# Kernel optimization log

Hardware: AMD Instinct MI355X
Metric: run time of the kernel (lower is better)

Reference implementation:

```python
import jax, jax.numpy as jnp
import numpy as np
import math

V = 32000      # vocab_size
CTX = 1025     # context_length (S = CTX-1)
L = 4          # num_layers
D = 1024       # hidden_dim
H = 16         # heads
DH = D // H    # head_dim
FF = 4 * D
B = 2
PAD = 3        # padding_idx / tokenizer.pad_id()


def setup_inputs() -> dict:
    key = jax.random.key(0)
    ks = jax.random.split(key, 16)
    g = lambda k, shape: jax.random.normal(k, shape, dtype=jnp.float32) * 0.02
    text = jax.random.randint(ks[0], (B, CTX), 0, V)
    emb = g(ks[1], (V, D)).at[PAD].set(0.0)   # nn.Embedding with padding_idx=3
    u = g(ks[2], (H, DH))
    v = g(ks[3], (H, DH))
    Wq = g(ks[4], (L, D, D))
    Wk = g(ks[5], (L, D, D))
    Wv = g(ks[6], (L, D, D))
    Wr = g(ks[7], (L, D, D))
    Wfc = g(ks[8], (L, D, D))
    bfc = jnp.zeros((L, D), jnp.float32)
    ln1g = jnp.ones((L, D), jnp.float32); ln1b = jnp.zeros((L, D), jnp.float32)
    ln2g = jnp.ones((L, D), jnp.float32); ln2b = jnp.zeros((L, D), jnp.float32)
    W1 = g(ks[9], (L, D, FF)); b1 = jnp.zeros((L, FF), jnp.float32)
    W2 = g(ks[10], (L, FF, D)); b2 = jnp.zeros((L, D), jnp.float32)
    lnfg = jnp.ones((D,), jnp.float32); lnfb = jnp.zeros((D,), jnp.float32)
    Wlm = g(ks[11], (D, V)); blm = jnp.zeros((V,), jnp.float32)
    return dict(text=text, emb=emb, u=u, v=v, Wq=Wq, Wk=Wk, Wv=Wv, Wr=Wr,
                Wfc=Wfc, bfc=bfc, ln1g=ln1g, ln1b=ln1b, ln2g=ln2g, ln2b=ln2b,
                W1=W1, b1=b1, W2=W2, b2=b2, lnfg=lnfg, lnfb=lnfb, Wlm=Wlm, blm=blm)


def _ln(x, g, b, eps=1e-5):
    m = x.mean(-1, keepdims=True)
    va = ((x - m) ** 2).mean(-1, keepdims=True)
    return (x - m) / jnp.sqrt(va + eps) * g + b


def _rel_shift(x):
    # Transformer-XL relative shift: pad a zero column, reshape, drop first row.
    b, h, s, r = x.shape
    xp = jnp.pad(x, ((0, 0), (0, 0), (0, 0), (1, 0)))     # (b,h,s,r+1)
    xp = xp.reshape(b, h, r + 1, s)
    return xp[:, :, 1:, :].reshape(b, h, s, r)


def _forward(text, emb, u, v, Wq, Wk, Wv, Wr, Wfc, bfc, ln1g, ln1b, ln2g, ln2b,
             W1, b1, W2, b2, lnfg, lnfb, Wlm, blm):
    ip = text[:, :-1]                 # ip_text = text[:, :-1]
    S = ip.shape[1]
    x = emb[ip]                       # (B,S,D)
    # PositionalEmbedding over Transformer-XL positions [S-1 .. 0]
    pos = jnp.arange(S - 1, -1, -1, dtype=jnp.float32)
    inv_freq = 1.0 / (10000.0 ** (jnp.arange(0, D, 2, dtype=jnp.float32) / D))
    sinu = pos[:, None] * inv_freq[None, :]
    rel = jnp.concatenate([jnp.sin(sinu), jnp.cos(sinu)], axis=-1)  # (S,D)
    # get_mask: causal triu OR pad-token rows
    causal = jnp.triu(jnp.ones((S, S), dtype=bool), 1)
    pad = (ip == PAD)
    mask = (pad[:, :, None] | causal[None]) [:, None, :, :]        # (B,1,S,S)
    full_row = mask.all(-1, keepdims=True)                          # fully-masked rows -> NaN-fill 0
    scale = 1.0 / math.sqrt(DH)
    for l in range(L):
        xn = _ln(x, ln1g[l], ln1b[l])
        q = (xn @ Wq[l]).reshape(B, S, H, DH).transpose(0, 2, 1, 3)   # (B,H,S,DH)
        k = (xn @ Wk[l]).reshape(B, S, H, DH).transpose(0, 2, 1, 3)
        vv = (xn @ Wv[l]).reshape(B, S, H, DH).transpose(0, 2, 1, 3)
        r = (rel @ Wr[l]).reshape(S, H, DH).transpose(1, 0, 2)        # (H,S,DH)
        term_AC = jnp.einsum('bhqd,bhkd->bhqk', q + u[None, :, None, :], k)
        term_BD = jnp.einsum('bhqd,hkd->bhqk', q + v[None, :, None, :], r)
        term_BD = _rel_shift(term_BD)
        scores = (term_AC + term_BD) * scale
        scores = jnp.where(mask, -1e30, scores)
        aw = jax.nn.softmax(scores, axis=-1)
        aw = jnp.where(full_row, 0.0, aw)                              # NaN -> 0 masking
        o = jnp.einsum('bhqk,bhkd->bhqd', aw, vv).transpose(0, 2, 1, 3).reshape(B, S, D)
        o = o @ Wfc[l] + bfc[l] + xn                                   # fc(out) + attn-input residual
        x = x + o                                                      # block residual
        h = _ln(x, ln2g[l], ln2b[l])
        f = jax.nn.gelu(h @ W1[l] + b1[l])
        f = jax.nn.gelu(f @ W2[l] + b2[l])
        x = x + f
    xf = _ln(x, lnfg, lnfb)
    return xf @ Wlm + blm                                              # (B,S,V) logits


def reference(text, emb, u, v, Wq, Wk, Wv, Wr, Wfc, bfc, ln1g, ln1b, ln2g, ln2b,
              W1, b1, W2, b2, lnfg, lnfb, Wlm, blm):
    return _forward(text, emb, u, v, Wq, Wk, Wv, Wr, Wfc, bfc, ln1g, ln1b,
                    ln2g, ln2b, W1, b1, W2, b2, lnfg, lnfb, Wlm, blm)
```

## Files before the change

kernel.cpp:

```cpp
#include <hip/hip_runtime.h>
#include <stdint.h>

#define S_ 1024
#define D_ 1024
#define H_ 16
#define DH_ 64
#define FF_ 4096
#define B_ 2
#define V_ 32000
#define CTX_ 1025
#define PAD_ 3

typedef unsigned short u16;
typedef __attribute__((ext_vector_type(8))) short bf16x8;
typedef __attribute__((ext_vector_type(4))) float f32x4;

enum { EPI_BF16 = 0, EPI_QKV = 1, EPI_FC = 2, EPI_GELU_BF16 = 3, EPI_GELU_RES = 4, EPI_BIAS_F32 = 5 };

__device__ __forceinline__ u16 f2bf(float f) {
  unsigned u = __float_as_uint(f);
  return (u16)((u + 0x7FFFu + ((u >> 16) & 1u)) >> 16);
}

__device__ __forceinline__ float bf2f(u16 v) {
  return __uint_as_float(((unsigned)v) << 16);
}

__device__ __forceinline__ float gelu_f(float x) {
  float t = tanhf(0.7978845608028654f * (x + 0.044715f * x * x * x));
  return 0.5f * x * (1.0f + t);
}

__device__ __forceinline__ void glds16(const void* g, void* l) {
  __builtin_amdgcn_global_load_lds(
      (const __attribute__((address_space(1))) unsigned int*)g,
      (__attribute__((address_space(3))) unsigned int*)l,
      16, 0, 0);
}

__global__ __launch_bounds__(256) void embed_gather(const int* __restrict__ text,
                                                    const float* __restrict__ emb,
                                                    float* __restrict__ x) {
  int row = blockIdx.x;
  int b = row >> 10, s = row & 1023;
  int id = text[b * CTX_ + s];
  float4 v = ((const float4*)(emb + (size_t)id * D_))[threadIdx.x];
  ((float4*)(x + (size_t)row * D_))[threadIdx.x] = v;
}

__global__ __launch_bounds__(256) void rel_enc(u16* __restrict__ rel) {
  int i = blockIdx.x;
  float pos = (float)(S_ - 1 - i);
  for (int t = threadIdx.x; t < 512; t += 256) {
    float invf = exp2f(-(float)t * (13.287712379549449f / 512.0f));
    float ang = pos * invf;
    rel[(size_t)i * D_ + t] = f2bf(sinf(ang));
    rel[(size_t)i * D_ + 512 + t] = f2bf(cosf(ang));
  }
}

__global__ __launch_bounds__(256) void wconv_t(const float* __restrict__ src,
                                               u16* __restrict__ dst, int K, int N) {
  src += (size_t)blockIdx.z * K * N;
  dst += (size_t)blockIdx.z * K * N;
  __shared__ float tile[32][33];
  int n0 = blockIdx.x * 32, k0 = blockIdx.y * 32;
  for (int idx = threadIdx.x; idx < 1024; idx += 256) {
    int r = idx >> 5, c = idx & 31;
    tile[r][c] = src[(size_t)(k0 + r) * N + n0 + c];
  }
  __syncthreads();
  for (int idx = threadIdx.x; idx < 1024; idx += 256) {
    int r = idx >> 5, c = idx & 31;
    dst[(size_t)(n0 + r) * K + k0 + c] = f2bf(tile[c][r]);
  }
}

__global__ __launch_bounds__(256) void wconv4_k(const float* __restrict__ sq,
                                                const float* __restrict__ sk,
                                                const float* __restrict__ sv,
                                                const float* __restrict__ sf,
                                                u16* __restrict__ dqkv,
                                                u16* __restrict__ dfc) {
  const int z = blockIdx.z;
  const float* src = (z == 0) ? sq : (z == 1) ? sk : (z == 2) ? sv : sf;
  u16* dst = (z < 3) ? dqkv + (size_t)z * 1024 * 1024 : dfc;
  __shared__ float tile[32][33];
  int n0 = blockIdx.x * 32, k0 = blockIdx.y * 32;
  for (int idx = threadIdx.x; idx < 1024; idx += 256) {
    int r = idx >> 5, c = idx & 31;
    tile[r][c] = src[(size_t)(k0 + r) * 1024 + n0 + c];
  }
  __syncthreads();
  for (int idx = threadIdx.x; idx < 1024; idx += 256) {
    int r = idx >> 5, c = idx & 31;
    dst[(size_t)(n0 + r) * 1024 + k0 + c] = f2bf(tile[c][r]);
  }
}

__global__ __launch_bounds__(256) void layernorm_k(const float* __restrict__ x,
                                                   const float* __restrict__ g,
                                                   const float* __restrict__ bb,
                                                   float* __restrict__ outf,
                                                   u16* __restrict__ outb) {
  int row = blockIdx.x, tid = threadIdx.x;
  const float* xr = x + (size_t)row * D_;
  float4 v = ((const float4*)xr)[tid];
  float s = v.x + v.y + v.z + v.w;
  float s2 = v.x * v.x + v.y * v.y + v.z * v.z + v.w * v.w;
  __shared__ float red[8];
#pragma unroll
  for (int off = 32; off > 0; off >>= 1) { s += __shfl_xor(s, off); s2 += __shfl_xor(s2, off); }
  if ((tid & 63) == 0) { red[tid >> 6] = s; red[4 + (tid >> 6)] = s2; }
  __syncthreads();
  s = red[0] + red[1] + red[2] + red[3];
  s2 = red[4] + red[5] + red[6] + red[7];
  float mean = s * (1.0f / D_);
  float var = s2 * (1.0f / D_) - mean * mean;
  float rstd = rsqrtf(var + 1e-5f);
  float4 gv = ((const float4*)g)[tid];
  float4 bv = ((const float4*)bb)[tid];
  float y0 = (v.x - mean) * rstd * gv.x + bv.x;
  float y1 = (v.y - mean) * rstd * gv.y + bv.y;
  float y2 = (v.z - mean) * rstd * gv.z + bv.z;
  float y3 = (v.w - mean) * rstd * gv.w + bv.w;
  if (outf) ((float4*)(outf + (size_t)row * D_))[tid] = make_float4(y0, y1, y2, y3);
  ((ushort4*)(outb + (size_t)row * D_))[tid] = make_ushort4(f2bf(y0), f2bf(y1), f2bf(y2), f2bf(y3));
}

__device__ __forceinline__ void epi_one(int mode, float v, int row, int col, int ldc,
                                        void* C0p, void* C1p, void* C2p, void* C3p,
                                        const float* bias0, const float* bias1,
                                        const float* res0) {
  if (mode == EPI_QKV) {
    int seg = col >> 10, c = col & 1023;
    size_t idx = (size_t)row * 1024 + c;
    if (seg == 0) {
      ((u16*)C0p)[idx] = f2bf(v + bias0[c]);
      ((u16*)C1p)[idx] = f2bf(v + bias1[c]);
    } else if (seg == 1) {
      ((u16*)C2p)[idx] = f2bf(v);
    } else {
      ((u16*)C3p)[idx] = f2bf(v);
    }
    return;
  }
  size_t idx = (size_t)row * ldc + col;
  float b0 = bias0 ? bias0[col] : 0.0f;
  if (mode == EPI_BF16) {
    ((u16*)C0p)[idx] = f2bf(v);
  } else if (mode == EPI_FC) {
    float* C0 = (float*)C0p;
    C0[idx] = C0[idx] + v + b0 + res0[idx];
  } else if (mode == EPI_GELU_BF16) {
    ((u16*)C0p)[idx] = f2bf(gelu_f(v + b0));
  } else if (mode == EPI_GELU_RES) {
    float* C0 = (float*)C0p;
    C0[idx] = C0[idx] + gelu_f(v + b0);
  } else {
    ((float*)C0p)[idx] = v + b0;
  }
}

__global__ __launch_bounds__(256) void gemm_bt(const u16* __restrict__ A,
                                               const u16* __restrict__ Bt,
                                               int M, int N, int K,
                                               void* __restrict__ C0p, void* __restrict__ C1p,
                                               void* __restrict__ C2p, void* __restrict__ C3p,
                                               const float* __restrict__ bias0,
                                               const float* __restrict__ bias1,
                                               const float* __restrict__ res0,
                                               int ldc, int mode) {
  __shared__ u16 lA[128 * 64];
  __shared__ u16 lB[128 * 64];
  const int tid = threadIdx.x;
  const int wave = tid >> 6, lane = tid & 63;
  unsigned gx = gridDim.x, gy = gridDim.y;
  unsigned nwg = gx * gy;
  unsigned bx = blockIdx.x, by = blockIdx.y;
  if ((nwg & 7u) == 0u) {
    unsigned lin = by * gx + bx;
    unsigned v = (lin & 7u) * (nwg >> 3) + (lin >> 3);
    bx = v / gy;
    by = v - bx * gy;
  }
  const int i0 = by * 128, j0 = bx * 128;
  const int wm = wave & 1, wn = wave >> 1;
  const int m_lane = lane & 15, quad = lane >> 4;

  f32x4 acc[4][4] = {};

  const u16* Ab = A + (size_t)i0 * K;
  const u16* Bb = Bt + (size_t)j0 * K;
  const int sr = lane >> 3;
  const int sc = ((lane & 7) ^ sr) * 8;

  for (int k0 = 0; k0 < K; k0 += 64) {
#pragma unroll
    for (int c = 0; c < 4; c++) {
      int row = wave * 32 + c * 8 + sr;
      glds16(Ab + (size_t)row * K + k0 + sc, lA + (size_t)(wave * 32 + c * 8) * 64);
      glds16(Bb + (size_t)row * K + k0 + sc, lB + (size_t)(wave * 32 + c * 8) * 64);
    }
    __syncthreads();
    bf16x8 af[4], bfr[4];
#pragma unroll
    for (int t = 0; t < 4; t++) {
      int ra = wm * 64 + t * 16 + m_lane;
      int rb_ = wn * 64 + t * 16 + m_lane;
      af[t]  = *(const bf16x8*)(lA + ra * 64 + ((quad ^ (ra & 7)) * 8));
      bfr[t] = *(const bf16x8*)(lB + rb_ * 64 + ((quad ^ (rb_ & 7)) * 8));
    }
#pragma unroll
    for (int mt = 0; mt < 4; mt++)
#pragma unroll
      for (int nt = 0; nt < 4; nt++)
        acc[mt][nt] = __builtin_amdgcn_mfma_f32_16x16x32_bf16(af[mt], bfr[nt], acc[mt][nt], 0, 0, 0);
#pragma unroll
    for (int t = 0; t < 4; t++) {
      int ra = wm * 64 + t * 16 + m_lane;
      int rb_ = wn * 64 + t * 16 + m_lane;
      af[t]  = *(const bf16x8*)(lA + ra * 64 + (((4 + quad) ^ (ra & 7)) * 8));
      bfr[t] = *(const bf16x8*)(lB + rb_ * 64 + (((4 + quad) ^ (rb_ & 7)) * 8));
    }
#pragma unroll
    for (int mt = 0; mt < 4; mt++)
#pragma unroll
      for (int nt = 0; nt < 4; nt++)
        acc[mt][nt] = __builtin_amdgcn_mfma_f32_16x16x32_bf16(af[mt], bfr[nt], acc[mt][nt], 0, 0, 0);
    __syncthreads();
  }

#pragma unroll
  for (int mt = 0; mt < 4; mt++) {
#pragma unroll
    for (int nt = 0; nt < 4; nt++) {
      int col = j0 + wn * 64 + nt * 16 + m_lane;
#pragma unroll
      for (int r = 0; r < 4; r++) {
        int row = i0 + wm * 64 + mt * 16 + quad * 4 + r;
        epi_one(mode, acc[mt][nt][r], row, col, ldc, C0p, C1p, C2p, C3p, bias0, bias1, res0);
      }
    }
  }
}

__global__ __launch_bounds__(256) void gemm_bt64(const u16* __restrict__ A,
                                                 const u16* __restrict__ Bt,
                                                 int M, int N, int K,
                                                 void* __restrict__ C0p, void* __restrict__ C1p,
                                                 void* __restrict__ C2p, void* __restrict__ C3p,
                                                 const float* __restrict__ bias0,
                                                 const float* __restrict__ bias1,
                                                 const float* __restrict__ res0,
                                                 int ldc, int mode) {
  __shared__ u16 lA[64 * 64];
  __shared__ u16 lB[128 * 64];
  const int tid = threadIdx.x;
  const int wave = tid >> 6, lane = tid & 63;
  unsigned gx = gridDim.x, gy = gridDim.y;
  unsigned nwg = gx * gy;
  unsigned bx = blockIdx.x, by = blockIdx.y;
  if ((nwg & 7u) == 0u) {
    unsigned lin = by * gx + bx;
    unsigned v = (lin & 7u) * (nwg >> 3) + (lin >> 3);
    by = v / gx;
    bx = v - by * gx;
  }
  const int i0 = by * 64, j0 = bx * 128;
  const int m_lane = lane & 15, quad = lane >> 4;

  f32x4 acc[4][2] = {};

  const u16* Ab = A + (size_t)i0 * K;
  const u16* Bb = Bt + (size_t)j0 * K;
  const int sr = lane >> 3;
  const int sc = ((lane & 7) ^ sr) * 8;

  for (int k0 = 0; k0 < K; k0 += 64) {
#pragma unroll
    for (int c = 0; c < 2; c++) {
      int row = wave * 16 + c * 8 + sr;
      glds16(Ab + (size_t)row * K + k0 + sc, lA + (size_t)(wave * 16 + c * 8) * 64);
    }
#pragma unroll
    for (int c = 0; c < 4; c++) {
      int row = wave * 32 + c * 8 + sr;
      glds16(Bb + (size_t)row * K + k0 + sc, lB + (size_t)(wave * 32 + c * 8) * 64);
    }
    __syncthreads();
    bf16x8 af[4], bfr[2];
#pragma unroll
    for (int t = 0; t < 4; t++) {
      int ra = t * 16 + m_lane;
      af[t] = *(const bf16x8*)(lA + ra * 64 + ((quad ^ (ra & 7)) * 8));
    }
#pragma unroll
    for (int t = 0; t < 2; t++) {
      int rb_ = wave * 32 + t * 16 + m_lane;
      bfr[t] = *(const bf16x8*)(lB + rb_ * 64 + ((quad ^ (rb_ & 7)) * 8));
    }
#pragma unroll
    for (int mt = 0; mt < 4; mt++)
#pragma unroll
      for (int nt = 0; nt < 2; nt++)
        acc[mt][nt] = __builtin_amdgcn_mfma_f32_16x16x32_bf16(af[mt], bfr[nt], acc[mt][nt], 0, 0, 0);
#pragma unroll
    for (int t = 0; t < 4; t++) {
      int ra = t * 16 + m_lane;
      af[t] = *(const bf16x8*)(lA + ra * 64 + (((4 + quad) ^ (ra & 7)) * 8));
    }
#pragma unroll
    for (int t = 0; t < 2; t++) {
      int rb_ = wave * 32 + t * 16 + m_lane;
      bfr[t] = *(const bf16x8*)(lB + rb_ * 64 + (((4 + quad) ^ (rb_ & 7)) * 8));
    }
#pragma unroll
    for (int mt = 0; mt < 4; mt++)
#pragma unroll
      for (int nt = 0; nt < 2; nt++)
        acc[mt][nt] = __builtin_amdgcn_mfma_f32_16x16x32_bf16(af[mt], bfr[nt], acc[mt][nt], 0, 0, 0);
    __syncthreads();
  }

#pragma unroll
  for (int mt = 0; mt < 4; mt++) {
#pragma unroll
    for (int nt = 0; nt < 2; nt++) {
      int col = j0 + wave * 32 + nt * 16 + m_lane;
#pragma unroll
      for (int r = 0; r < 4; r++) {
        int row = i0 + mt * 16 + quad * 4 + r;
        epi_one(mode, acc[mt][nt][r], row, col, ldc, C0p, C1p, C2p, C3p, bias0, bias1, res0);
      }
    }
  }
}

__global__ __launch_bounds__(256) void attn_score(const u16* __restrict__ qu,
                                                  const u16* __restrict__ qv,
                                                  const u16* __restrict__ kk,
                                                  const u16* __restrict__ rb,
                                                  float* __restrict__ scores) {
  __shared__ u16 sBD[64][132];
  const int cIdx = blockIdx.x, bh = blockIdx.y;
  int ti = (int)((sqrtf(8.0f * (float)cIdx + 1.0f) - 1.0f) * 0.5f);
  while ((ti + 1) * (ti + 2) / 2 <= cIdx) ti++;
  while (ti * (ti + 1) / 2 > cIdx) ti--;
  const int tj = cIdx - ti * (ti + 1) / 2;
  const int b = bh >> 4, h = bh & 15;
  const int tid = threadIdx.x, wave = tid >> 6, lane = tid & 63;
  const int m_lane = lane & 15, quad = lane >> 4;
  const int i0 = ti * 64, j0 = tj * 64;
  const int T0 = 15 - (ti - tj);
  const bool hasT1 = (T0 < 15);

  const u16* Qu = qu + ((size_t)(b * S_ + i0 + wave * 16 + m_lane)) * D_ + h * DH_ + quad * 8;
  const u16* Qv = qv + ((size_t)(b * S_ + i0 + wave * 16 + m_lane)) * D_ + h * DH_ + quad * 8;
  bf16x8 a0 = *(const bf16x8*)(Qu);
  bf16x8 a1 = *(const bf16x8*)(Qu + 32);
  bf16x8 c0 = *(const bf16x8*)(Qv);
  bf16x8 c1 = *(const bf16x8*)(Qv + 32);

  const u16* Kb = kk + ((size_t)(b * S_ + j0)) * D_ + h * DH_;
  const u16* R0 = rb + ((size_t)(T0 * 64)) * 4096 + h * DH_;
  const u16* R1 = R0 + (size_t)64 * 4096;

  f32x4 ac_[4] = {}, bd0_[4] = {}, bd1_[4] = {};
#pragma unroll
  for (int nt = 0; nt < 4; nt++) {
    const u16* kr = Kb + (size_t)(nt * 16 + m_lane) * D_ + quad * 8;
    bf16x8 kb0 = *(const bf16x8*)(kr);
    bf16x8 kb1 = *(const bf16x8*)(kr + 32);
    ac_[nt] = __builtin_amdgcn_mfma_f32_16x16x32_bf16(a0, kb0, ac_[nt], 0, 0, 0);
    ac_[nt] = __builtin_amdgcn_mfma_f32_16x16x32_bf16(a1, kb1, ac_[nt], 0, 0, 0);
    const u16* rr = R0 + (size_t)(nt * 16 + m_lane) * 4096 + quad * 8;
    bf16x8 rb0 = *(const bf16x8*)(rr);
    bf16x8 rb1 = *(const bf16x8*)(rr + 32);
    bd0_[nt] = __builtin_amdgcn_mfma_f32_16x16x32_bf16(c0, rb0, bd0_[nt], 0, 0, 0);
    bd0_[nt] = __builtin_amdgcn_mfma_f32_16x16x32_bf16(c1, rb1, bd0_[nt], 0, 0, 0);
    if (hasT1) {
      const u16* r2 = R1 + (size_t)(nt * 16 + m_lane) * 4096 + quad * 8;
      bf16x8 rc0 = *(const bf16x8*)(r2);
      bf16x8 rc1 = *(const bf16x8*)(r2 + 32);
      bd1_[nt] = __builtin_amdgcn_mfma_f32_16x16x32_bf16(c0, rc0, bd1_[nt], 0, 0, 0);
      bd1_[nt] = __builtin_amdgcn_mfma_f32_16x16x32_bf16(c1, rc1, bd1_[nt], 0, 0, 0);
    }
  }

#pragma unroll
  for (int nt = 0; nt < 4; nt++) {
    int col = nt * 16 + m_lane;
#pragma unroll
    for (int r = 0; r < 4; r++) {
      int row = wave * 16 + quad * 4 + r;
      sBD[row][col] = f2bf(bd0_[nt][r]);
      sBD[row][64 + col] = hasT1 ? f2bf(bd1_[nt][r]) : (u16)0;
    }
  }
  __syncthreads();

  float* C = scores + (size_t)bh * S_ * S_ + (size_t)i0 * S_ + j0;
#pragma unroll
  for (int nt = 0; nt < 4; nt++) {
    int jl = nt * 16 + m_lane;
#pragma unroll
    for (int r = 0; r < 4; r++) {
      int il = wave * 16 + quad * 4 + r;
      int tloc = jl - il + 63;
      C[(size_t)il * S_ + jl] = ac_[nt][r] + bf2f(sBD[il][tloc]);
    }
  }
}

__global__ __launch_bounds__(256) void attn_gemm(const u16* __restrict__ A, int lda,
                                                 const u16* __restrict__ Bt, int ldb,
                                                 float* __restrict__ Cf, u16* __restrict__ Cb,
                                                 int K, int mode) {
  const int ti = blockIdx.x, tj = blockIdx.y, bh = blockIdx.z;
  if (mode == 0 && tj > ti) return;
  if (mode == 1 && ti + tj < 15) return;
  const int b = bh >> 4, h = bh & 15;
  __shared__ u16 lA[64 * 64];
  __shared__ u16 lB[64 * 64];
  const int tid = threadIdx.x, wave = tid >> 6, lane = tid & 63;
  const int m_lane = lane & 15, quad = lane >> 4;
  const int i0 = ti * 64, j0 = tj * 64;

  size_t aoff, boff;
  if (mode == 0)      { aoff = (size_t)b * S_ * D_ + h * DH_; boff = (size_t)b * S_ * D_ + h * DH_; }
  else if (mode == 1) { aoff = (size_t)b * S_ * D_ + h * DH_; boff = (size_t)h * DH_; }
  else                { aoff = (size_t)bh * S_ * S_;          boff = (size_t)bh * DH_ * S_; }
  const u16* Ap = A + aoff + (size_t)i0 * lda;
  const u16* Bp = Bt + boff + (mode == 2 ? (size_t)0 : (size_t)j0 * ldb);

  f32x4 acc[4] = {};
  const int sr = lane >> 3;
  const int sc = ((lane & 7) ^ sr) * 8;

  const int Kend = (mode == 2) ? (ti + 1) * 64 : K;
  for (int k0 = 0; k0 < Kend; k0 += 64) {
#pragma unroll
    for (int c = 0; c < 2; c++) {
      int row = wave * 16 + c * 8 + sr;
      glds16(Ap + (size_t)row * lda + k0 + sc, lA + (size_t)(wave * 16 + c * 8) * 64);
      glds16(Bp + (size_t)row * ldb + k0 + sc, lB + (size_t)(wave * 16 + c * 8) * 64);
    }
    __syncthreads();
    int ra = wave * 16 + m_lane;
    bf16x8 a0 = *(const bf16x8*)(lA + ra * 64 + ((quad ^ (ra & 7)) * 8));
    bf16x8 a1 = *(const bf16x8*)(lA + ra * 64 + (((4 + quad) ^ (ra & 7)) * 8));
#pragma unroll
    for (int nt = 0; nt < 4; nt++) {
      int rb_ = nt * 16 + m_lane;
      bf16x8 b0 = *(const bf16x8*)(lB + rb_ * 64 + ((quad ^ (rb_ & 7)) * 8));
      bf16x8 b1 = *(const bf16x8*)(lB + rb_ * 64 + (((4 + quad) ^ (rb_ & 7)) * 8));
      acc[nt] = __builtin_amdgcn_mfma_f32_16x16x32_bf16(a0, b0, acc[nt], 0, 0, 0);
      acc[nt] = __builtin_amdgcn_mfma_f32_16x16x32_bf16(a1, b1, acc[nt], 0, 0, 0);
    }
    __syncthreads();
  }

  if (mode == 0) {
    float* C = Cf + (size_t)bh * S_ * S_;
#pragma unroll
    for (int nt = 0; nt < 4; nt++) {
      int col = j0 + nt * 16 + m_lane;
#pragma unroll
      for (int r = 0; r < 4; r++) {
        int row = i0 + wave * 16 + quad * 4 + r;
        C[(size_t)row * S_ + col] = acc[nt][r];
      }
    }
  } else if (mode == 1) {
    float* C = Cf + (size_t)bh * S_ * S_;
#pragma unroll
    for (int nt = 0; nt < 4; nt++) {
      int t = j0 + nt * 16 + m_lane;
#pragma unroll
      for (int r = 0; r < 4; r++) {
        int row = i0 + wave * 16 + quad * 4 + r;
        int j = row + t - (S_ - 1);
        if (j >= 0) C[(size_t)row * S_ + j] += acc[nt][r];
      }
    }
  } else {
    u16* C = Cb + (size_t)b * S_ * D_ + h * DH_;
#pragma unroll
    for (int nt = 0; nt < 4; nt++) {
      int col = nt * 16 + m_lane;
#pragma unroll
      for (int r = 0; r < 4; r++) {
        int row = i0 + wave * 16 + quad * 4 + r;
        C[(size_t)row * D_ + col] = f2bf(acc[nt][r]);
      }
    }
  }
}

__global__ __launch_bounds__(256) void softmax_k(const float* __restrict__ scores,
                                                 u16* __restrict__ aw,
                                                 const int* __restrict__ text) {
  const int i = blockIdx.x, bh = blockIdx.y, b = bh >> 4;
  const float* s = scores + ((size_t)bh * S_ + i) * S_;
  u16* o = aw + ((size_t)bh * S_ + i) * S_;
  const int tid = threadIdx.x, wave = tid >> 6, lane = tid & 63;
  const int n = i + 1;
  const int jmax = ((i >> 6) + 1) << 6;
  const int j0 = tid * 4;
  if (text[b * CTX_ + i] == PAD_) {
    if (j0 < jmax) ((ushort4*)o)[tid] = make_ushort4(0, 0, 0, 0);
    return;
  }
  const float scale = 0.125f;
  float4 sv = make_float4(0.f, 0.f, 0.f, 0.f);
  if (j0 < jmax) sv = ((const float4*)s)[tid];
  float e0 = (j0 + 0 < n) ? sv.x * scale : -3e38f;
  float e1 = (j0 + 1 < n) ? sv.y * scale : -3e38f;
  float e2 = (j0 + 2 < n) ? sv.z * scale : -3e38f;
  float e3 = (j0 + 3 < n) ? sv.w * scale : -3e38f;
  float mx = fmaxf(fmaxf(e0, e1), fmaxf(e2, e3));
  __shared__ float red[8];
#pragma unroll
  for (int off = 32; off > 0; off >>= 1) mx = fmaxf(mx, __shfl_xor(mx, off));
  if (lane == 0) red[wave] = mx;
  __syncthreads();
  mx = fmaxf(fmaxf(red[0], red[1]), fmaxf(red[2], red[3]));
  float p0 = __expf(e0 - mx);
  float p1 = __expf(e1 - mx);
  float p2 = __expf(e2 - mx);
  float p3 = __expf(e3 - mx);
  float sum = p0 + p1 + p2 + p3;
#pragma unroll
  for (int off = 32; off > 0; off >>= 1) sum += __shfl_xor(sum, off);
  if (lane == 0) red[4 + wave] = sum;
  __syncthreads();
  sum = red[4] + red[5] + red[6] + red[7];
  float inv = 1.0f / sum;
  if (j0 < jmax)
    ((ushort4*)o)[tid] = make_ushort4(f2bf(p0 * inv), f2bf(p1 * inv), f2bf(p2 * inv), f2bf(p3 * inv));
}

__global__ __launch_bounds__(256) void v_transpose(const u16* __restrict__ v,
                                                   u16* __restrict__ vT) {
  int bh = blockIdx.y, b = bh >> 4, h = bh & 15;
  int j0 = blockIdx.x * 64;
  __shared__ u16 tile[64][65];
  for (int idx = threadIdx.x; idx < 4096; idx += 256) {
    int jj = idx >> 6, d = idx & 63;
    tile[jj][d] = v[(size_t)(b * S_ + j0 + jj) * D_ + h * DH_ + d];
  }
  __syncthreads();
  for (int idx = threadIdx.x; idx < 4096; idx += 256) {
    int d = idx >> 6, jj = idx & 63;
    vT[((size_t)bh * DH_ + d) * S_ + j0 + jj] = tile[jj][d];
  }
}

extern "C" void kernel_launch(void* const* d_in, const int* in_sizes, int n_in,
                              void* d_out, int out_size, void* d_ws, size_t ws_size,
                              hipStream_t stream) {
  (void)in_sizes; (void)n_in; (void)out_size;
  const int* text = (const int*)d_in[0];
  const float* emb = (const float*)d_in[1];
  const float* u_in = (const float*)d_in[2];
  const float* v_in = (const float*)d_in[3];
  const float* Wq = (const float*)d_in[4];
  const float* Wk = (const float*)d_in[5];
  const float* Wv = (const float*)d_in[6];
  const float* Wr = (const float*)d_in[7];
  const float* Wfc = (const float*)d_in[8];
  const float* bfc = (const float*)d_in[9];
  const float* ln1g = (const float*)d_in[10];
  const float* ln1b = (const float*)d_in[11];
  const float* ln2g = (const float*)d_in[12];
  const float* ln2b = (const float*)d_in[13];
  const float* W1 = (const float*)d_in[14];
  const float* b1 = (const float*)d_in[15];
  const float* W2 = (const float*)d_in[16];
  const float* b2 = (const float*)d_in[17];
  const float* lnfg = (const float*)d_in[18];
  const float* lnfb = (const float*)d_in[19];
  const float* Wlm = (const float*)d_in[20];
  const float* blm = (const float*)d_in[21];
  float* out = (float*)d_out;

  char* w = (char*)d_ws;
  size_t off = 0;
  auto alloc = [&](size_t bytes) -> void* {
    void* p = w + off;
    off += (bytes + 255) & ~(size_t)255;
    return p;
  };
  float* x      = (float*)alloc(2048ull * 1024 * 4);
  float* xnf    = (float*)alloc(2048ull * 1024 * 4);
  u16* xnb      = (u16*)alloc(2048ull * 1024 * 2);
  u16* relb     = (u16*)alloc(1024ull * 1024 * 2);
  u16* wqkvt    = (u16*)alloc(3072ull * 1024 * 2);
  u16* wrt_all  = (u16*)alloc(4096ull * 1024 * 2);
  u16* wfct     = (u16*)alloc(1024ull * 1024 * 2);
  u16* w1t      = (u16*)alloc(4096ull * 1024 * 2);
  u16* w2t      = (u16*)alloc(4096ull * 1024 * 2);
  u16* wlmt     = (u16*)alloc(32000ull * 1024 * 2);
  u16* qu       = (u16*)alloc(2048ull * 1024 * 2);
  u16* qv       = (u16*)alloc(2048ull * 1024 * 2);
  u16* kk       = (u16*)alloc(2048ull * 1024 * 2);
  u16* vv       = (u16*)alloc(2048ull * 1024 * 2);
  u16* vT       = (u16*)alloc(2048ull * 1024 * 2);
  u16* rb_all   = (u16*)alloc(1024ull * 4096 * 2);
  float* scores = (float*)alloc(32ull * 1024 * 1024 * 4);
  u16* aw       = (u16*)alloc(32ull * 1024 * 1024 * 2);
  u16* o_       = (u16*)alloc(2048ull * 1024 * 2);
  u16* f1       = (u16*)alloc(2048ull * 4096 * 2);
  if (off > ws_size) return;

  dim3 blk(256);
  embed_gather<<<2048, blk, 0, stream>>>(text, emb, x);
  rel_enc<<<1024, blk, 0, stream>>>(relb);
  wconv_t<<<dim3(1000, 32), blk, 0, stream>>>(Wlm, wlmt, 1024, 32000);
  wconv_t<<<dim3(32, 32, 4), blk, 0, stream>>>(Wr, wrt_all, 1024, 1024);
  gemm_bt<<<dim3(32, 8), blk, 0, stream>>>(relb, wrt_all, 1024, 4096, 1024,
                                           rb_all, nullptr, nullptr, nullptr,
                                           nullptr, nullptr, nullptr, 4096, EPI_BF16);

  for (int l = 0; l < 4; l++) {
    const size_t dd = 1048576;
    wconv4_k<<<dim3(32, 32, 4), blk, 0, stream>>>(Wq + l * dd, Wk + l * dd, Wv + l * dd,
                                                  Wfc + l * dd, wqkvt, wfct);
    wconv_t<<<dim3(128, 32), blk, 0, stream>>>(W1 + l * 4ull * dd, w1t, 1024, 4096);
    wconv_t<<<dim3(32, 128), blk, 0, stream>>>(W2 + l * 4ull * dd, w2t, 4096, 1024);

    layernorm_k<<<2048, blk, 0, stream>>>(x, ln1g + l * 1024, ln1b + l * 1024, xnf, xnb);

    gemm_bt<<<dim3(24, 16), blk, 0, stream>>>(xnb, wqkvt, 2048, 3072, 1024,
                                              qu, qv, kk, vv, u_in, v_in, nullptr, 1024, EPI_QKV);
    v_transpose<<<dim3(16, 32), blk, 0, stream>>>(vv, vT);

    attn_score<<<dim3(136, 32), blk, 0, stream>>>(qu, qv, kk, rb_all + (size_t)l * 1024, scores);
    softmax_k<<<dim3(1024, 32), blk, 0, stream>>>(scores, aw, text);
    attn_gemm<<<dim3(16, 1, 32), blk, 0, stream>>>(aw, 1024, vT, 1024, nullptr, o_, 1024, 2);

    gemm_bt64<<<dim3(8, 32), blk, 0, stream>>>(o_, wfct, 2048, 1024, 1024,
                                               x, nullptr, nullptr, nullptr,
                                               bfc + l * 1024, nullptr, xnf, 1024, EPI_FC);
    layernorm_k<<<2048, blk, 0, stream>>>(x, ln2g + l * 1024, ln2b + l * 1024, nullptr, xnb);
    gemm_bt<<<dim3(32, 16), blk, 0, stream>>>(xnb, w1t, 2048, 4096, 1024,
                                              f1, nullptr, nullptr, nullptr,
                                              b1 + l * 4096, nullptr, nullptr, 4096, EPI_GELU_BF16);
    gemm_bt64<<<dim3(8, 32), blk, 0, stream>>>(f1, w2t, 2048, 1024, 4096,
                                               x, nullptr, nullptr, nullptr,
                                               b2 + l * 1024, nullptr, nullptr, 1024, EPI_GELU_RES);
  }

  layernorm_k<<<2048, blk, 0, stream>>>(x, lnfg, lnfb, nullptr, xnb);
  gemm_bt<<<dim3(250, 16), blk, 0, stream>>>(xnb, wlmt, 2048, 32000, 1024,
                                             out, nullptr, nullptr, nullptr,
                                             blm, nullptr, nullptr, 32000, EPI_BIAS_F32);
}
```

Measured before the change: 2.311 ms.

## Fuse relative-position attention into a flash-style kernel and retile LM head GEMM

Replaces the separate score, softmax and AV kernels with a single online-softmax kernel per 64-row query tile. It also writes V directly in transposed layout from the QKV epilogue, removing the transpose kernel and the large fp32 score and bf16 probability buffers. The LM-head GEMM switches to a new 128x128 tile kernel with a K-step of 32. Only 16x32 blocks launch for attention, so occupancy drops and work per block is unbalanced across causal rows, though the grid interleaves long and short tiles to spread it.

```diff
diff --git a/kernel.cpp b/kernel.cpp
--- a/kernel.cpp
+++ b/kernel.cpp
@@ -134,13 +134,15 @@
                                         const float* res0) {
   if (mode == EPI_QKV) {
     int seg = col >> 10, c = col & 1023;
-    size_t idx = (size_t)row * 1024 + c;
     if (seg == 0) {
+      size_t idx = (size_t)row * 1024 + c;
       ((u16*)C0p)[idx] = f2bf(v + bias0[c]);
       ((u16*)C1p)[idx] = f2bf(v + bias1[c]);
     } else if (seg == 1) {
-      ((u16*)C2p)[idx] = f2bf(v);
+      ((u16*)C2p)[(size_t)row * 1024 + c] = f2bf(v);
     } else {
+      int d = c & 63, hh = c >> 6;
+      size_t idx = (((size_t)((row >> 10) * 16 + hh) * 64 + d) << 10) + (row & 1023);
       ((u16*)C3p)[idx] = f2bf(v);
     }
     return;
@@ -159,6 +161,73 @@
     C0[idx] = C0[idx] + gelu_f(v + b0);
   } else {
     ((float*)C0p)[idx] = v + b0;
+  }
+}
+
+__global__ __launch_bounds__(256) void gemm_bt32(const u16* __restrict__ A,
+                                                 const u16* __restrict__ Bt,
+                                                 int M, int N, int K,
+                                                 void* __restrict__ C0p, void* __restrict__ C1p,
+                                                 void* __restrict__ C2p, void* __restrict__ C3p,
+                                                 const float* __restrict__ bias0,
+                                                 const float* __restrict__ bias1,
+                                                 const float* __restrict__ res0,
+                                                 int ldc, int mode) {
+  __shared__ u16 lA[128 * 32];
+  __shared__ u16 lB[128 * 32];
+  const int tid = threadIdx.x;
+  const int wave = tid >> 6, lane = tid & 63;
+  unsigned gx = gridDim.x, gy = gridDim.y;
+  unsigned nwg = gx * gy;
+  unsigned bx = blockIdx.x, by = blockIdx.y;
+  if ((nwg & 7u) == 0u) {
+    unsigned lin = by * gx + bx;
+    unsigned v = (lin & 7u) * (nwg >> 3) + (lin >> 3);
+    bx = v / gy;
+    by = v - bx * gy;
+  }
+  const int i0 = by * 128, j0 = bx * 128;
+  const int wm = wave & 1, wn = wave >> 1;
+  const int m_lane = lane & 15, quad = lane >> 4;
+
+  f32x4 acc[4][4] = {};
+
+  const u16* Ab = A + (size_t)i0 * K;
+  const u16* Bb = Bt + (size_t)j0 * K;
+  const int r0 = wave * 32 + (lane >> 2);
+  const int cb = (lane & 3) * 8;
+
+  for (int k0 = 0; k0 < K; k0 += 32) {
+    glds16(Ab + (size_t)r0 * K + k0 + cb, lA + wave * 1024);
+    glds16(Ab + (size_t)(r0 + 16) * K + k0 + cb, lA + wave * 1024 + 512);
+    glds16(Bb + (size_t)r0 * K + k0 + cb, lB + wave * 1024);
+    glds16(Bb + (size_t)(r0 + 16) * K + k0 + cb, lB + wave * 1024 + 512);
+    __syncthreads();
+    bf16x8 af[4], bfr[4];
+#pragma unroll
+    for (int t = 0; t < 4; t++) {
+      af[t] = *(const bf16x8*)(lA + (wm * 64 + t * 16 + m_lane) * 32 + quad * 8);
+      bfr[t] = *(const bf16x8*)(lB + (wn * 64 + t * 16 + m_lane) * 32 + quad * 8);
+    }
+#pragma unroll
+    for (int mt = 0; mt < 4; mt++)
+#pragma unroll
+      for (int nt = 0; nt < 4; nt++)
+        acc[mt][nt] = __builtin_amdgcn_mfma_f32_16x16x32_bf16(af[mt], bfr[nt], acc[mt][nt], 0, 0, 0);
+    __syncthreads();
+  }
+
+#pragma unroll
+  for (int mt = 0; mt < 4; mt++) {
+#pragma unroll
+    for (int nt = 0; nt < 4; nt++) {
+      int col = j0 + wn * 64 + nt * 16 + m_lane;
+#pragma unroll
+      for (int r = 0; r < 4; r++) {
+        int row = i0 + wm * 64 + mt * 16 + quad * 4 + r;
+        epi_one(mode, acc[mt][nt][r], row, col, ldc, C0p, C1p, C2p, C3p, bias0, bias1, res0);
+      }
+    }
   }
 }
 
@@ -337,23 +406,21 @@
   }
 }
 
-__global__ __launch_bounds__(256) void attn_score(const u16* __restrict__ qu,
+__global__ __launch_bounds__(256) void attn_flash(const u16* __restrict__ qu,
                                                   const u16* __restrict__ qv,
                                                   const u16* __restrict__ kk,
                                                   const u16* __restrict__ rb,
-                                                  float* __restrict__ scores) {
+                                                  const u16* __restrict__ vT,
+                                                  const int* __restrict__ text,
+                                                  u16* __restrict__ o_) {
   __shared__ u16 sBD[64][132];
-  const int cIdx = blockIdx.x, bh = blockIdx.y;
-  int ti = (int)((sqrtf(8.0f * (float)cIdx + 1.0f) - 1.0f) * 0.5f);
-  while ((ti + 1) * (ti + 2) / 2 <= cIdx) ti++;
-  while (ti * (ti + 1) / 2 > cIdx) ti--;
-  const int tj = cIdx - ti * (ti + 1) / 2;
+  __shared__ u16 sP[64][72];
+  const int bx = blockIdx.x, bh = blockIdx.y;
+  const int ti = (bx & 1) ? (bx >> 1) : (15 - (bx >> 1));
   const int b = bh >> 4, h = bh & 15;
   const int tid = threadIdx.x, wave = tid >> 6, lane = tid & 63;
   const int m_lane = lane & 15, quad = lane >> 4;
-  const int i0 = ti * 64, j0 = tj * 64;
-  const int T0 = 15 - (ti - tj);
-  const bool hasT1 = (T0 < 15);
+  const int i0 = ti * 64;
 
   const u16* Qu = qu + ((size_t)(b * S_ + i0 + wave * 16 + m_lane)) * D_ + h * DH_ + quad * 8;
   const u16* Qv = qv + ((size_t)(b * S_ + i0 + wave * 16 + m_lane)) * D_ + h * DH_ + quad * 8;
@@ -362,198 +429,124 @@
   bf16x8 c0 = *(const bf16x8*)(Qv);
   bf16x8 c1 = *(const bf16x8*)(Qv + 32);
 
-  const u16* Kb = kk + ((size_t)(b * S_ + j0)) * D_ + h * DH_;
-  const u16* R0 = rb + ((size_t)(T0 * 64)) * 4096 + h * DH_;
-  const u16* R1 = R0 + (size_t)64 * 4096;
-
-  f32x4 ac_[4] = {}, bd0_[4] = {}, bd1_[4] = {};
-#pragma unroll
-  for (int nt = 0; nt < 4; nt++) {
-    const u16* kr = Kb + (size_t)(nt * 16 + m_lane) * D_ + quad * 8;
-    bf16x8 kb0 = *(const bf16x8*)(kr);
-    bf16x8 kb1 = *(const bf16x8*)(kr + 32);
-    ac_[nt] = __builtin_amdgcn_mfma_f32_16x16x32_bf16(a0, kb0, ac_[nt], 0, 0, 0);
-    ac_[nt] = __builtin_amdgcn_mfma_f32_16x16x32_bf16(a1, kb1, ac_[nt], 0, 0, 0);
-    const u16* rr = R0 + (size_t)(nt * 16 + m_lane) * 4096 + quad * 8;
-    bf16x8 rb0 = *(const bf16x8*)(rr);
-    bf16x8 rb1 = *(const bf16x8*)(rr + 32);
-    bd0_[nt] = __builtin_amdgcn_mfma_f32_16x16x32_bf16(c0, rb0, bd0_[nt], 0, 0, 0);
-    bd0_[nt] = __builtin_amdgcn_mfma_f32_16x16x32_bf16(c1, rb1, bd0_[nt], 0, 0, 0);
-    if (hasT1) {
-      const u16* r2 = R1 + (size_t)(nt * 16 + m_lane) * 4096 + quad * 8;
-      bf16x8 rc0 = *(const bf16x8*)(r2);
-      bf16x8 rc1 = *(const bf16x8*)(r2 + 32);
-      bd1_[nt] = __builtin_amdgcn_mfma_f32_16x16x32_bf16(c0, rc0, bd1_[nt], 0, 0, 0);
-      bd1_[nt] = __builtin_amdgcn_mfma_f32_16x16x32_bf16(c1, rc1, bd1_[nt], 0, 0, 0);
-    }
-  }
-
-#pragma unroll
-  for (int nt = 0; nt < 4; nt++) {
-    int col = nt * 16 + m_lane;
-#pragma unroll
-    for (int r = 0; r < 4; r++) {
-      int row = wave * 16 + quad * 4 + r;
-      sBD[row][col] = f2bf(bd0_[nt][r]);
-      sBD[row][64 + col] = hasT1 ? f2bf(bd1_[nt][r]) : (u16)0;
-    }
-  }
-  __syncthreads();
-
-  float* C = scores + (size_t)bh * S_ * S_ + (size_t)i0 * S_ + j0;
-#pragma unroll
-  for (int nt = 0; nt < 4; nt++) {
-    int jl = nt * 16 + m_lane;
-#pragma unroll
-    for (int r = 0; r < 4; r++) {
-      int il = wave * 16 + quad * 4 + r;
-      int tloc = jl - il + 63;
-      C[(size_t)il * S_ + jl] = ac_[nt][r] + bf2f(sBD[il][tloc]);
-    }
-  }
-}
-
-__global__ __launch_bounds__(256) void attn_gemm(const u16* __restrict__ A, int lda,
-                                                 const u16* __restrict__ Bt, int ldb,
-                                                 float* __restrict__ Cf, u16* __restrict__ Cb,
-                                                 int K, int mode) {
-  const int ti = blockIdx.x, tj = blockIdx.y, bh = blockIdx.z;
-  if (mode == 0 && tj > ti) return;
-  if (mode == 1 && ti + tj < 15) return;
-  const int b = bh >> 4, h = bh & 15;
-  __shared__ u16 lA[64 * 64];
-  __shared__ u16 lB[64 * 64];
-  const int tid = threadIdx.x, wave = tid >> 6, lane = tid & 63;
-  const int m_lane = lane & 15, quad = lane >> 4;
-  const int i0 = ti * 64, j0 = tj * 64;
-
-  size_t aoff, boff;
-  if (mode == 0)      { aoff = (size_t)b * S_ * D_ + h * DH_; boff = (size_t)b * S_ * D_ + h * DH_; }
-  else if (mode == 1) { aoff = (size_t)b * S_ * D_ + h * DH_; boff = (size_t)h * DH_; }
-  else                { aoff = (size_t)bh * S_ * S_;          boff = (size_t)bh * DH_ * S_; }
-  const u16* Ap = A + aoff + (size_t)i0 * lda;
-  const u16* Bp = Bt + boff + (mode == 2 ? (size_t)0 : (size_t)j0 * ldb);
-
-  f32x4 acc[4] = {};
-  const int sr = lane >> 3;
-  const int sc = ((lane & 7) ^ sr) * 8;
-
-  const int Kend = (mode == 2) ? (ti + 1) * 64 : K;
-  for (int k0 = 0; k0 < Kend; k0 += 64) {
-#pragma unroll
-    for (int c = 0; c < 2; c++) {
-      int row = wave * 16 + c * 8 + sr;
-      glds16(Ap + (size_t)row * lda + k0 + sc, lA + (size_t)(wave * 16 + c * 8) * 64);
-      glds16(Bp + (size_t)row * ldb + k0 + sc, lB + (size_t)(wave * 16 + c * 8) * 64);
-    }
-    __syncthreads();
-    int ra = wave * 16 + m_lane;
-    bf16x8 a0 = *(const bf16x8*)(lA + ra * 64 + ((quad ^ (ra & 7)) * 8));
-    bf16x8 a1 = *(const bf16x8*)(lA + ra * 64 + (((4 + quad) ^ (ra & 7)) * 8));
+  const u16* vTb = vT + (size_t)bh * DH_ * S_;
+
+  f32x4 oacc[4] = {};
+  float m_[4] = {-3e38f, -3e38f, -3e38f, -3e38f};
+  float l_[4] = {0.f, 0.f, 0.f, 0.f};
+
+  for (int tj = 0; tj <= ti; tj++) {
+    const int j0 = tj * 64;
+    const int T0 = 15 - (ti - tj);
+    const bool hasT1 = (T0 < 15);
+    const u16* Kb = kk + ((size_t)(b * S_ + j0)) * D_ + h * DH_;
+    const u16* R0 = rb + ((size_t)(T0 * 64)) * 4096 + h * DH_;
+    const u16* R1 = R0 + (size_t)64 * 4096;
+
+    f32x4 ac_[4] = {}, bd0_[4] = {}, bd1_[4] = {};
+    __builtin_amdgcn_s_setprio(1);
 #pragma unroll
     for (int nt = 0; nt < 4; nt++) {
-      int rb_ = nt * 16 + m_lane;
-      bf16x8 b0 = *(const bf16x8*)(lB + rb_ * 64 + ((quad ^ (rb_ & 7)) * 8));
-      bf16x8 b1 = *(const bf16x8*)(lB + rb_ * 64 + (((4 + quad) ^ (rb_ & 7)) * 8));
-      acc[nt] = __builtin_amdgcn_mfma_f32_16x16x32_bf16(a0, b0, acc[nt], 0, 0, 0);
-      acc[nt] = __builtin_amdgcn_mfma_f32_16x16x32_bf16(a1, b1, acc[nt], 0, 0, 0);
-    }
-    __syncthreads();
-  }
-
-  if (mode == 0) {
-    float* C = Cf + (size_t)bh * S_ * S_;
-#pragma unroll
-    for (int nt = 0; nt < 4; nt++) {
-      int col = j0 + nt * 16 + m_lane;
-#pragma unroll
-      for (int r = 0; r < 4; r++) {
-        int row = i0 + wave * 16 + quad * 4 + r;
-        C[(size_t)row * S_ + col] = acc[nt][r];
+      const u16* kr = Kb + (size_t)(nt * 16 + m_lane) * D_ + quad * 8;
+      bf16x8 kb0 = *(const bf16x8*)(kr);
+      bf16x8 kb1 = *(const bf16x8*)(kr + 32);
+      ac_[nt] = __builtin_amdgcn_mfma_f32_16x16x32_bf16(a0, kb0, ac_[nt], 0, 0, 0);
+      ac_[nt] = __builtin_amdgcn_mfma_f32_16x16x32_bf16(a1, kb1, ac_[nt], 0, 0, 0);
+      const u16* rr = R0 + (size_t)(nt * 16 + m_lane) * 4096 + quad * 8;
+      bf16x8 rb0 = *(const bf16x8*)(rr);
+      bf16x8 rb1 = *(const bf16x8*)(rr + 32);
+      bd0_[nt] = __builtin_amdgcn_mfma_f32_16x16x32_bf16(c0, rb0, bd0_[nt], 0, 0, 0);
+      bd0_[nt] = __builtin_amdgcn_mfma_f32_16x16x32_bf16(c1, rb1, bd0_[nt], 0, 0, 0);
+      if (hasT1) {
+        const u16* r2 = R1 + (size_t)(nt * 16 + m_lane) * 4096 + quad * 8;
+        bf16x8 rc0 = *(const bf16x8*)(r2);
+        bf16x8 rc1 = *(const bf16x8*)(r2 + 32);
+        bd1_[nt] = __builtin_amdgcn_mfma_f32_16x16x32_bf16(c0, rc0, bd1_[nt], 0, 0, 0);
+        bd1_[nt] = __builtin_amdgcn_mfma_f32_16x16x32_bf16(c1, rc1, bd1_[nt], 0, 0, 0);
       }
     }
-  } else if (mode == 1) {
-    float* C = Cf + (size_t)bh * S_ * S_;
-#pragma unroll
-    for (int nt = 0; nt < 4; nt++) {
-      int t = j0 + nt * 16 + m_lane;
-#pragma unroll
-      for (int r = 0; r < 4; r++) {
-        int row = i0 + wave * 16 + quad * 4 + r;
-        int j = row + t - (S_ - 1);
-        if (j >= 0) C[(size_t)row * S_ + j] += acc[nt][r];
-      }
-    }
-  } else {
-    u16* C = Cb + (size_t)b * S_ * D_ + h * DH_;
+    __builtin_amdgcn_s_setprio(0);
+
 #pragma unroll
     for (int nt = 0; nt < 4; nt++) {
       int col = nt * 16 + m_lane;
 #pragma unroll
       for (int r = 0; r < 4; r++) {
-        int row = i0 + wave * 16 + quad * 4 + r;
-        C[(size_t)row * D_ + col] = f2bf(acc[nt][r]);
+        int row = wave * 16 + quad * 4 + r;
+        sBD[row][col] = f2bf(bd0_[nt][r]);
+        sBD[row][64 + col] = hasT1 ? f2bf(bd1_[nt][r]) : (u16)0;
       }
     }
-  }
-}
-
-__global__ __launch_bounds__(256) void softmax_k(const float* __restrict__ scores,
-                                                 u16* __restrict__ aw,
-                                                 const int* __restrict__ text) {
-  const int i = blockIdx.x, bh = blockIdx.y, b = bh >> 4;
-  const float* s = scores + ((size_t)bh * S_ + i) * S_;
-  u16* o = aw + ((size_t)bh * S_ + i) * S_;
-  const int tid = threadIdx.x, wave = tid >> 6, lane = tid & 63;
-  const int n = i + 1;
-  const int jmax = ((i >> 6) + 1) << 6;
-  const int j0 = tid * 4;
-  if (text[b * CTX_ + i] == PAD_) {
-    if (j0 < jmax) ((ushort4*)o)[tid] = make_ushort4(0, 0, 0, 0);
-    return;
-  }
-  const float scale = 0.125f;
-  float4 sv = make_float4(0.f, 0.f, 0.f, 0.f);
-  if (j0 < jmax) sv = ((const float4*)s)[tid];
-  float e0 = (j0 + 0 < n) ? sv.x * scale : -3e38f;
-  float e1 = (j0 + 1 < n) ? sv.y * scale : -3e38f;
-  float e2 = (j0 + 2 < n) ? sv.z * scale : -3e38f;
-  float e3 = (j0 + 3 < n) ? sv.w * scale : -3e38f;
-  float mx = fmaxf(fmaxf(e0, e1), fmaxf(e2, e3));
-  __shared__ float red[8];
-#pragma unroll
-  for (int off = 32; off > 0; off >>= 1) mx = fmaxf(mx, __shfl_xor(mx, off));
-  if (lane == 0) red[wave] = mx;
-  __syncthreads();
-  mx = fmaxf(fmaxf(red[0], red[1]), fmaxf(red[2], red[3]));
-  float p0 = __expf(e0 - mx);
-  float p1 = __expf(e1 - mx);
-  float p2 = __expf(e2 - mx);
-  float p3 = __expf(e3 - mx);
-  float sum = p0 + p1 + p2 + p3;
-#pragma unroll
-  for (int off = 32; off > 0; off >>= 1) sum += __shfl_xor(sum, off);
-  if (lane == 0) red[4 + wave] = sum;
-  __syncthreads();
-  sum = red[4] + red[5] + red[6] + red[7];
-  float inv = 1.0f / sum;
-  if (j0 < jmax)
-    ((ushort4*)o)[tid] = make_ushort4(f2bf(p0 * inv), f2bf(p1 * inv), f2bf(p2 * inv), f2bf(p3 * inv));
-}
-
-__global__ __launch_bounds__(256) void v_transpose(const u16* __restrict__ v,
-                                                   u16* __restrict__ vT) {
-  int bh = blockIdx.y, b = bh >> 4, h = bh & 15;
-  int j0 = blockIdx.x * 64;
-  __shared__ u16 tile[64][65];
-  for (int idx = threadIdx.x; idx < 4096; idx += 256) {
-    int jj = idx >> 6, d = idx & 63;
-    tile[jj][d] = v[(size_t)(b * S_ + j0 + jj) * D_ + h * DH_ + d];
-  }
-  __syncthreads();
-  for (int idx = threadIdx.x; idx < 4096; idx += 256) {
-    int d = idx >> 6, jj = idx & 63;
-    vT[((size_t)bh * DH_ + d) * S_ + j0 + jj] = tile[jj][d];
+
+    float p_[4][4];
+#pragma unroll
+    for (int nt = 0; nt < 4; nt++) {
+      int jl = nt * 16 + m_lane;
+#pragma unroll
+      for (int r = 0; r < 4; r++) {
+        int il = wave * 16 + quad * 4 + r;
+        float s = (ac_[nt][r] + bf2f(sBD[il][jl - il + 63])) * 0.125f;
+        if (ti == tj && jl > il) s = -3e38f;
+        p_[nt][r] = s;
+      }
+    }
+
+#pragma unroll
+    for (int r = 0; r < 4; r++) {
+      float t = fmaxf(fmaxf(p_[0][r], p_[1][r]), fmaxf(p_[2][r], p_[3][r]));
+      t = fmaxf(t, __shfl_xor(t, 1));
+      t = fmaxf(t, __shfl_xor(t, 2));
+      t = fmaxf(t, __shfl_xor(t, 4));
+      t = fmaxf(t, __shfl_xor(t, 8));
+      float mn = fmaxf(m_[r], t);
+      float corr = __expf(m_[r] - mn);
+      m_[r] = mn;
+      float ts = 0.f;
+#pragma unroll
+      for (int nt = 0; nt < 4; nt++) {
+        float p = __expf(p_[nt][r] - mn);
+        p_[nt][r] = p;
+        ts += p;
+      }
+      ts += __shfl_xor(ts, 1);
+      ts += __shfl_xor(ts, 2);
+      ts += __shfl_xor(ts, 4);
+      ts += __shfl_xor(ts, 8);
+      l_[r] = l_[r] * corr + ts;
+#pragma unroll
+      for (int nt = 0; nt < 4; nt++) oacc[nt][r] *= corr;
+    }
+
+#pragma unroll
+    for (int nt = 0; nt < 4; nt++) {
+      int col = nt * 16 + m_lane;
+#pragma unroll
+      for (int r = 0; r < 4; r++)
+        sP[wave * 16 + quad * 4 + r][col] = f2bf(p_[nt][r]);
+    }
+    bf16x8 pa0 = *(const bf16x8*)(&sP[wave * 16 + m_lane][quad * 8]);
+    bf16x8 pa1 = *(const bf16x8*)(&sP[wave * 16 + m_lane][32 + quad * 8]);
+    __builtin_amdgcn_s_setprio(1);
+#pragma unroll
+    for (int nt = 0; nt < 4; nt++) {
+      const u16* vr = vTb + (size_t)(nt * 16 + m_lane) * S_ + j0 + quad * 8;
+      bf16x8 bv0 = *(const bf16x8*)(vr);
+      bf16x8 bv1 = *(const bf16x8*)(vr + 32);
+      oacc[nt] = __builtin_amdgcn_mfma_f32_16x16x32_bf16(pa0, bv0, oacc[nt], 0, 0, 0);
+      oacc[nt] = __builtin_amdgcn_mfma_f32_16x16x32_bf16(pa1, bv1, oacc[nt], 0, 0, 0);
+    }
+    __builtin_amdgcn_s_setprio(0);
+  }
+
+  u16* Ob = o_ + (size_t)b * S_ * D_ + h * DH_;
+#pragma unroll
+  for (int r = 0; r < 4; r++) {
+    int row = i0 + wave * 16 + quad * 4 + r;
+    bool pad = (text[b * CTX_ + row] == PAD_);
+    float inv = pad ? 0.0f : (1.0f / l_[r]);
+#pragma unroll
+    for (int nt = 0; nt < 4; nt++)
+      Ob[(size_t)row * D_ + nt * 16 + m_lane] = f2bf(oacc[nt][r] * inv);
   }
 }
 
@@ -605,11 +598,8 @@
   u16* qu       = (u16*)alloc(2048ull * 1024 * 2);
   u16* qv       = (u16*)alloc(2048ull * 1024 * 2);
   u16* kk       = (u16*)alloc(2048ull * 1024 * 2);
-  u16* vv       = (u16*)alloc(2048ull * 1024 * 2);
   u16* vT       = (u16*)alloc(2048ull * 1024 * 2);
   u16* rb_all   = (u16*)alloc(1024ull * 4096 * 2);
-  float* scores = (float*)alloc(32ull * 1024 * 1024 * 4);
-  u16* aw       = (u16*)alloc(32ull * 1024 * 1024 * 2);
   u16* o_       = (u16*)alloc(2048ull * 1024 * 2);
   u16* f1       = (u16*)alloc(2048ull * 4096 * 2);
   if (off > ws_size) return;
@@ -633,12 +623,10 @@
     layernorm_k<<<2048, blk, 0, stream>>>(x, ln1g + l * 1024, ln1b + l * 1024, xnf, xnb);
 
     gemm_bt<<<dim3(24, 16), blk, 0, stream>>>(xnb, wqkvt, 2048, 3072, 1024,
-                                              qu, qv, kk, vv, u_in, v_in, nullptr, 1024, EPI_QKV);
-    v_transpose<<<dim3(16, 32), blk, 0, stream>>>(vv, vT);
-
-    attn_score<<<dim3(136, 32), blk, 0, stream>>>(qu, qv, kk, rb_all + (size_t)l * 1024, scores);
-    softmax_k<<<dim3(1024, 32), blk, 0, stream>>>(scores, aw, text);
-    attn_gemm<<<dim3(16, 1, 32), blk, 0, stream>>>(aw, 1024, vT, 1024, nullptr, o_, 1024, 2);
+                                              qu, qv, kk, vT, u_in, v_in, nullptr, 1024, EPI_QKV);
+
+    attn_flash<<<dim3(16, 32), blk, 0, stream>>>(qu, qv, kk, rb_all + (size_t)l * 1024,
+                                                 vT, text, o_);
 
     gemm_bt64<<<dim3(8, 32), blk, 0, stream>>>(o_, wfct, 2048, 1024, 1024,
                                                x, nullptr, nullptr, nullptr,
@@ -653,7 +641,7 @@
   }
 
   layernorm_k<<<2048, blk, 0, stream>>>(x, lnfg, lnfb, nullptr, xnb);
-  gemm_bt<<<dim3(250, 16), blk, 0, stream>>>(xnb, wlmt, 2048, 32000, 1024,
-                                             out, nullptr, nullptr, nullptr,
-                                             blm, nullptr, nullptr, 32000, EPI_BIAS_F32);
-}
+  gemm_bt32<<<dim3(250, 16), blk, 0, stream>>>(xnb, wlmt, 2048, 32000, 1024,
+                                               out, nullptr, nullptr, nullptr,
+                                               blm, nullptr, nullptr, 32000, EPI_BIAS_F32);
+}
```

Measured after the change: 2.419 ms. 1.05x slower.
